# Kernel optimization log

Measured on AMD Instinct MI355X. Metric: run time of the kernel, lower is better.

The kernel has to match this reference:

```python
import jax, jax.numpy as jnp
import numpy as np

N_NODES = 20000
N_EDGES = 100000
NODE_IN = 16
EDGE_IN = 10
LEAK = 0.1
EPS = 1e-5


def setup_inputs() -> dict:
    key = jax.random.key(0)
    ks = iter(jax.random.split(key, 40))

    def rn(shape, scale):
        return jax.random.normal(next(ks), shape, dtype=jnp.float32) * scale

    inp = {}
    inp["x"] = jax.random.normal(next(ks), (N_NODES, NODE_IN), dtype=jnp.float32)
    inp["e"] = jax.random.normal(next(ks), (N_EDGES, EDGE_IN), dtype=jnp.float32)
    inp["edge_index"] = jax.random.randint(next(ks), (2, N_EDGES), 0, N_NODES, dtype=jnp.int64)
    inp["xbatch"] = jnp.zeros((N_NODES,), dtype=jnp.int64)

    # BatchNorm affine params
    inp["bn_node_g"] = jnp.ones((NODE_IN,), jnp.float32)
    inp["bn_node_b"] = jnp.zeros((NODE_IN,), jnp.float32)
    inp["bn_edge_g"] = jnp.ones((EDGE_IN,), jnp.float32)
    inp["bn_edge_b"] = jnp.zeros((EDGE_IN,), jnp.float32)

    # nn1: Lin(10,16) -> LeakyReLU -> Lin(16, 16*32) -> LeakyReLU
    inp["nn1_w1"] = rn((EDGE_IN, 16), 0.3); inp["nn1_b1"] = jnp.zeros((16,), jnp.float32)
    inp["nn1_w2"] = rn((16, 16 * 32), 0.25); inp["nn1_b2"] = jnp.zeros((16 * 32,), jnp.float32)
    # nn2: Lin(10,32) -> LeakyReLU -> Lin(32, 32*64) -> LeakyReLU
    inp["nn2_w1"] = rn((EDGE_IN, 32), 0.3); inp["nn2_b1"] = jnp.zeros((32,), jnp.float32)
    inp["nn2_w2"] = rn((32, 32 * 64), 0.18); inp["nn2_b2"] = jnp.zeros((32 * 64,), jnp.float32)

    # NNConv root weights + biases
    inp["l1_root"] = rn((16, 32), 0.25); inp["l1_bias"] = jnp.zeros((32,), jnp.float32)
    inp["l2_root"] = rn((32, 64), 0.18); inp["l2_bias"] = jnp.zeros((64,), jnp.float32)

    # edge_pred_mlp: 138 -> 64 -> 32 -> 16 -> 8 -> 2
    dims = [2 * 64 + EDGE_IN, 64, 32, 16, 8, 2]
    for i in range(5):
        inp[f"mlp_w{i+1}"] = rn((dims[i], dims[i + 1]), 1.0 / np.sqrt(dims[i]))
        inp[f"mlp_b{i+1}"] = jnp.zeros((dims[i + 1],), jnp.float32)
    return inp


def _bn(v, g, b):
    # BatchNorm1d, training-mode batch statistics (biased variance), eps=1e-5
    m = v.mean(axis=0)
    var = v.var(axis=0)
    return (v - m) * jax.lax.rsqrt(var + EPS) * g + b


def _lrelu(v):
    return jax.nn.leaky_relu(v, LEAK)


def _nnconv(x, src, dst, e, w1, b1, w2, b2, root, bias, c_in, c_out):
    # edge MLP -> per-edge weight matrix [E, c_in, c_out]
    h = _lrelu(e @ w1 + b1)
    W = _lrelu(h @ w2 + b2).reshape(-1, c_in, c_out)
    # gather source features, per-edge matmul, scatter-add to targets
    msg = jnp.einsum("ei,eio->eo", x[src], W)
    agg = jax.ops.segment_sum(msg, dst, num_segments=x.shape[0])
    return agg + x @ root + bias


def reference(x, e, edge_index, xbatch,
              bn_node_g, bn_node_b, bn_edge_g, bn_edge_b,
              nn1_w1, nn1_b1, nn1_w2, nn1_b2,
              nn2_w1, nn2_b1, nn2_w2, nn2_b2,
              l1_root, l1_bias, l2_root, l2_bias,
              mlp_w1, mlp_b1, mlp_w2, mlp_b2, mlp_w3, mlp_b3,
              mlp_w4, mlp_b4, mlp_w5, mlp_b5):
    src, dst = edge_index[0], edge_index[1]
    e = _bn(e, bn_edge_g, bn_edge_b)
    x = _bn(x, bn_node_g, bn_node_b)
    x = _nnconv(x, src, dst, e, nn1_w1, nn1_b1, nn1_w2, nn1_b2, l1_root, l1_bias, 16, 32)
    x = _nnconv(x, src, dst, e, nn2_w1, nn2_b1, nn2_w2, nn2_b2, l2_root, l2_bias, 32, 64)
    # MetaLayer edge model: cat(source, target, edge_attr) -> MLP -> [E, 2]
    h = jnp.concatenate([x[src], x[dst], e], axis=1)
    h = _lrelu(h @ mlp_w1 + mlp_b1)
    h = _lrelu(h @ mlp_w2 + mlp_b2)
    h = _lrelu(h @ mlp_w3 + mlp_b3)
    h = _lrelu(h @ mlp_w4 + mlp_b4)
    edge_pred = h @ mlp_w5 + mlp_b5
    return edge_pred
```

## Files before the change

kernel.cpp:

```cpp
#include <hip/hip_runtime.h>
#include <cstdint>

#define N_NODES 20000
#define N_EDGES 100000
#define BN_EPS 1e-5f

typedef __attribute__((ext_vector_type(8))) short short8;
typedef __attribute__((ext_vector_type(4))) float floatx4;
typedef __attribute__((ext_vector_type(2))) float float2v;

__device__ __forceinline__ float lrelu(float v) { return fmaxf(v, 0.1f * v); }
__device__ __forceinline__ float4 ld4(const float* p) { return *reinterpret_cast<const float4*>(p); }
__device__ __forceinline__ float2 ld2(const float* p) { return *reinterpret_cast<const float2*>(p); }

__device__ __forceinline__ void atomAddF(float* p, float v) {
#if defined(__HIP_DEVICE_COMPILE__)
    unsafeAtomicAdd(p, v);
#else
    atomicAdd(p, v);
#endif
}

__device__ __forceinline__ unsigned short f2bf(float f) {
    union { float f; uint32_t u; } v; v.f = f;
    uint32_t r = v.u + 0x7fffu + ((v.u >> 16) & 1u);
    return (unsigned short)(r >> 16);
}
__device__ __forceinline__ uint32_t pack2(float a, float b) {
    return (uint32_t)f2bf(a) | ((uint32_t)f2bf(b) << 16);
}
__device__ __forceinline__ short8 pack8(float4 a, float4 b) {
    union { short8 s; uint32_t u[4]; } r;
    r.u[0] = pack2(a.x, a.y); r.u[1] = pack2(a.z, a.w);
    r.u[2] = pack2(b.x, b.y); r.u[3] = pack2(b.z, b.w);
    return r.s;
}

__device__ void stats10_dev(const float* __restrict__ v, int rows, float* __restrict__ out,
                            int blk, int nblk, float* sh) {
    if (threadIdx.x < 20) sh[threadIdx.x] = 0.f;
    __syncthreads();
    int nf2 = rows * 5;
    int stride = nblk * 256;
    int g = blk * 256 + threadIdx.x;
    int c2 = g % 5;
    float s0 = 0.f, s1 = 0.f, q0 = 0.f, q1 = 0.f;
    const float2* p = reinterpret_cast<const float2*>(v);
    for (int i = g; i < nf2; i += stride) {
        float2 t = p[i];
        s0 += t.x; s1 += t.y; q0 += t.x * t.x; q1 += t.y * t.y;
    }
    atomicAdd(&sh[2 * c2], s0);
    atomicAdd(&sh[2 * c2 + 1], s1);
    atomicAdd(&sh[10 + 2 * c2], q0);
    atomicAdd(&sh[10 + 2 * c2 + 1], q1);
    __syncthreads();
    if (threadIdx.x < 20) atomAddF(&out[threadIdx.x], sh[threadIdx.x]);
}

__device__ void stats16_dev(const float* __restrict__ v, int rows, float* __restrict__ out,
                            int blk, int nblk, float* sh) {
    if (threadIdx.x < 32) sh[threadIdx.x] = 0.f;
    __syncthreads();
    int nf4 = rows * 4;
    int stride = nblk * 256;
    int g = blk * 256 + threadIdx.x;
    int cg = (g & 3) * 4;
    float s[4] = {0.f, 0.f, 0.f, 0.f}, q[4] = {0.f, 0.f, 0.f, 0.f};
    const float4* p = reinterpret_cast<const float4*>(v);
    for (int i = g; i < nf4; i += stride) {
        float4 t = p[i];
        s[0] += t.x; s[1] += t.y; s[2] += t.z; s[3] += t.w;
        q[0] += t.x * t.x; q[1] += t.y * t.y; q[2] += t.z * t.z; q[3] += t.w * t.w;
    }
    #pragma unroll
    for (int off = 32; off >= 4; off >>= 1) {
        #pragma unroll
        for (int j = 0; j < 4; ++j) {
            s[j] += __shfl_down(s[j], off, 64);
            q[j] += __shfl_down(q[j], off, 64);
        }
    }
    if ((threadIdx.x & 63) < 4) {
        #pragma unroll
        for (int j = 0; j < 4; ++j) {
            atomicAdd(&sh[cg + j], s[j]);
            atomicAdd(&sh[16 + cg + j], q[j]);
        }
    }
    __syncthreads();
    if (threadIdx.x < 32) atomAddF(&out[threadIdx.x], sh[threadIdx.x]);
}

template<int CIN, int COUT, int H, int OCH>
__device__ void convpack_row(const float* __restrict__ w2, const float* __restrict__ b2,
                             char* __restrict__ pk, int r) {
    constexpr int NROW = CIN * OCH;
    constexpr int WB = NROW * 64;
    constexpr int PACKB = WB + NROW * 4;
    if (r >= CIN * COUT) return;
    int chunk = r / NROW;
    int rem = r % NROW;
    int i = rem / OCH, ol = rem % OCH;
    int n = i * COUT + chunk * OCH + ol;
    char* base = pk + (size_t)chunk * PACKB;
    uint32_t pkv[16];
    #pragma unroll
    for (int t = 0; t < 16; ++t) pkv[t] = 0;
    #pragma unroll
    for (int k = 0; k < H; k += 2)
        pkv[k >> 1] = pack2(w2[(size_t)k * (CIN * COUT) + n],
                            w2[(size_t)(k + 1) * (CIN * COUT) + n]);
    uint4* ob = reinterpret_cast<uint4*>(base);
    #pragma unroll
    for (int q = 0; q < 4; ++q)
        ob[(size_t)q * NROW + rem] = make_uint4(pkv[4 * q], pkv[4 * q + 1],
                                                pkv[4 * q + 2], pkv[4 * q + 3]);
    ((float*)(base + WB))[rem] = b2[n];
}

#define P1_S10 120
#define P1_S16 120
__global__ __launch_bounds__(256)
void prep1_kernel(const float* __restrict__ e, const float* __restrict__ x,
                  float* __restrict__ stats_e, float* __restrict__ stats_x,
                  const int* __restrict__ dst, int* __restrict__ counts,
                  const float* __restrict__ nn1_w2, const float* __restrict__ nn1_b2, char* __restrict__ cpack1,
                  const float* __restrict__ nn2_w2, const float* __restrict__ nn2_b2, char* __restrict__ cpack2,
                  const float* __restrict__ mw1, unsigned short* __restrict__ w1t,
                  const float* __restrict__ mw2, const float* __restrict__ mb2,
                  const float* __restrict__ mw3, const float* __restrict__ mb3,
                  const float* __restrict__ mw4, const float* __restrict__ mb4,
                  const float* __restrict__ mw5, const float* __restrict__ mb5,
                  float* __restrict__ mlpw)
{
    __shared__ float sh[32];
    int b = blockIdx.x;
    if (b < P1_S10) {
        stats10_dev(e, N_EDGES, stats_e, b, P1_S10, sh);
    } else if (b < P1_S10 + P1_S16) {
        stats16_dev(x, N_NODES, stats_x, b - P1_S10, P1_S16, sh);
    } else if (b < 631) {
        int i = (b - 240) * 256 + threadIdx.x;
        if (i < N_EDGES) atomicAdd(&counts[dst[i]], 1);
    } else if (b < 633) {
        convpack_row<16, 32, 16, 32>(nn1_w2, nn1_b2, cpack1, (b - 631) * 256 + threadIdx.x);
    } else if (b < 641) {
        convpack_row<32, 64, 32, 16>(nn2_w2, nn2_b2, cpack2, (b - 633) * 256 + threadIdx.x);
    } else {
        if (threadIdx.x < 64) {
            int o = threadIdx.x;
            for (int k = 0; k < 160; k += 2) {
                float a = (k < 138) ? mw1[(size_t)k * 64 + o] : 0.f;
                float c = (k + 1 < 138) ? mw1[(size_t)(k + 1) * 64 + o] : 0.f;
                *reinterpret_cast<uint32_t*>(w1t + (size_t)o * 160 + k) = pack2(a, c);
            }
        }
        for (int i = threadIdx.x; i < 2764; i += 256) {
            float v = 0.f;
            if (i < 2048) v = mw2[i];
            else if (i < 2560) v = mw3[i - 2048];
            else if (i < 2688) v = mw4[i - 2560];
            else if (i < 2704) v = mw5[i - 2688];
            else if (i < 2736) v = mb2[i - 2704];
            else if (i < 2752) v = mb3[i - 2736];
            else if (i < 2760) v = mb4[i - 2752];
            else if (i < 2762) v = mb5[i - 2760];
            mlpw[i] = v;
        }
    }
}

__global__ void scan_kernel(const int* __restrict__ counts, int* __restrict__ starts,
                            int* __restrict__ cursor, int n) {
    __shared__ int wsum[4];
    const int CH = (n + 255) / 256;
    int t = threadIdx.x;
    int lane = t & 63, wv = t >> 6;
    int lo = t * CH, hi = min(lo + CH, n);
    int s = 0;
    for (int i = lo; i < hi; ++i) s += counts[i];
    int v = s;
    #pragma unroll
    for (int off = 1; off < 64; off <<= 1) {
        int u = __shfl_up(v, off, 64);
        if (lane >= off) v += u;
    }
    if (lane == 63) wsum[wv] = v;
    __syncthreads();
    int woff = 0;
    for (int w = 0; w < wv; ++w) woff += wsum[w];
    int acc = woff + v - s;
    for (int i = lo; i < hi; ++i) {
        starts[i] = acc; cursor[i] = acc; acc += counts[i];
    }
}

#define P2_N16 1250
#define P2_SCAT 391
#define P2_HGEN 391
__global__ __launch_bounds__(256)
void prep2_kernel(const float* __restrict__ x, const float* __restrict__ stats_x,
                  const float* __restrict__ bn_node_g, const float* __restrict__ bn_node_b,
                  float* __restrict__ x_n,
                  const int* __restrict__ dst, int* __restrict__ cursor, int* __restrict__ epos,
                  const float* __restrict__ e, const float* __restrict__ stats_e,
                  const float* __restrict__ bn_edge_g, const float* __restrict__ bn_edge_b,
                  float* __restrict__ e_n,
                  const float* __restrict__ w1a, const float* __restrict__ b1a,
                  const float* __restrict__ w1b, const float* __restrict__ b1b,
                  unsigned short* __restrict__ h1, unsigned short* __restrict__ h2)
{
    int b = blockIdx.x;
    if (b < P2_N16) {
        int idx = b * 256 + threadIdx.x;
        if (idx >= N_NODES * 16) return;
        int c = idx & 15;
        float N = (float)N_NODES;
        float m = stats_x[c] / N;
        float var = stats_x[16 + c] / N - m * m;
        float sc = rsqrtf(var + BN_EPS) * bn_node_g[c];
        x_n[idx] = (x[idx] - m) * sc + bn_node_b[c];
    } else if (b < P2_N16 + P2_SCAT) {
        int i = (b - P2_N16) * 256 + threadIdx.x;
        if (i < N_EDGES) {
            int p = atomicAdd(&cursor[dst[i]], 1);
            epos[i] = p;
        }
    } else {
        int eg = (b - P2_N16 - P2_SCAT) * 256 + threadIdx.x;
        if (eg >= N_EDGES) return;
        float ev[10];
        float Ecnt = (float)N_EDGES;
        #pragma unroll
        for (int j = 0; j < 10; ++j) {
            float m = stats_e[j] / Ecnt;
            float var = stats_e[10 + j] / Ecnt - m * m;
            float sc = rsqrtf(var + BN_EPS) * bn_edge_g[j];
            ev[j] = (e[(size_t)eg * 10 + j] - m) * sc + bn_edge_b[j];
            e_n[(size_t)eg * 10 + j] = ev[j];
        }
        {
            uint32_t pk[16];
            #pragma unroll
            for (int t = 0; t < 16; ++t) pk[t] = 0;
            #pragma unroll
            for (int k = 0; k < 16; k += 2) {
                float a0 = b1a[k], a1 = b1a[k + 1];
                #pragma unroll
                for (int j = 0; j < 10; ++j) {
                    a0 += ev[j] * w1a[j * 16 + k];
                    a1 += ev[j] * w1a[j * 16 + k + 1];
                }
                pk[k >> 1] = pack2(lrelu(a0), lrelu(a1));
            }
            uint4* o = reinterpret_cast<uint4*>(h1 + (size_t)eg * 32);
            o[0] = make_uint4(pk[0], pk[1], pk[2], pk[3]);
            o[1] = make_uint4(pk[4], pk[5], pk[6], pk[7]);
            o[2] = make_uint4(pk[8], pk[9], pk[10], pk[11]);
            o[3] = make_uint4(pk[12], pk[13], pk[14], pk[15]);
        }
        {
            uint32_t pk[16];
            #pragma unroll
            for (int k = 0; k < 32; k += 2) {
                float a0 = b1b[k], a1 = b1b[k + 1];
                #pragma unroll
                for (int j = 0; j < 10; ++j) {
                    a0 += ev[j] * w1b[j * 32 + k];
                    a1 += ev[j] * w1b[j * 32 + k + 1];
                }
                pk[k >> 1] = pack2(lrelu(a0), lrelu(a1));
            }
            uint4* o = reinterpret_cast<uint4*>(h2 + (size_t)eg * 32);
            o[0] = make_uint4(pk[0], pk[1], pk[2], pk[3]);
            o[1] = make_uint4(pk[4], pk[5], pk[6], pk[7]);
            o[2] = make_uint4(pk[8], pk[9], pk[10], pk[11]);
            o[3] = make_uint4(pk[12], pk[13], pk[14], pk[15]);
        }
    }
}

template<int CIN, int COUT, int OCH, int NE, int IB>
__global__ __launch_bounds__(256, 4)
void conv_lds_kernel(const unsigned short* __restrict__ hbuf,
                     const char* __restrict__ pack,
                     const int* __restrict__ src,
                     const int* __restrict__ epos,
                     const float* __restrict__ xin,
                     float* __restrict__ msgbuf,
                     int n_edges)
{
    constexpr int NCH = COUT / OCH;
    constexpr int NROW = CIN * OCH;
    constexpr int WB = NROW * 64;
    constexpr int PACKB = WB + NROW * 4;
    constexpr int NOT = OCH / 16;
    __shared__ char smem[PACKB];

    int tid = threadIdx.x;
    int chunk = blockIdx.x % NCH;
    int eblk = blockIdx.x / NCH;

    {
        const uint4* g = reinterpret_cast<const uint4*>(pack + (size_t)chunk * PACKB);
        uint4* s = reinterpret_cast<uint4*>(smem);
        #pragma unroll 1
        for (int o = tid; o < PACKB / 16; o += 256) s[o] = g[o];
    }
    __syncthreads();

    int wv = tid >> 6, lane = tid & 63;
    int el = lane & 15, quad = lane >> 4;
    int g0 = (eblk * 4 + wv) * NE;
    if (g0 * 16 >= n_edges) return;

    const unsigned short* wlds = reinterpret_cast<const unsigned short*>(smem)
                                 + ((size_t)quad * NROW + el) * 8;
    const float* blds = reinterpret_cast<const float*>(smem + WB) + quad * 4;

    int sg[NE], slot[NE];
    short8 bfrag[NE];
    #pragma unroll
    for (int g = 0; g < NE; ++g) {
        int e0 = (g0 + g) * 16;
        int e = (e0 < n_edges) ? (e0 + el) : el;
        sg[g] = src[e];
        slot[g] = epos[e];
        bfrag[g] = *reinterpret_cast<const short8*>(hbuf + (size_t)e * 32 + quad * 8);
    }

    float2v msg0[NE][NOT], msg1[NE][NOT];
    #pragma unroll
    for (int g = 0; g < NE; ++g)
        #pragma unroll
        for (int t = 0; t < NOT; ++t) {
            msg0[g][t] = (float2v){0.f, 0.f};
            msg1[g][t] = (float2v){0.f, 0.f};
        }

    const float2v pt = {0.1f, 0.1f};

    #pragma unroll 1
    for (int ib = 0; ib < CIN / IB; ++ib) {
        float xs[NE][IB];
        #pragma unroll
        for (int g = 0; g < NE; ++g) {
            #pragma unroll
            for (int t = 0; t < IB; t += 4) {
                float4 v = ld4(xin + (size_t)sg[g] * CIN + ib * IB + t);
                xs[g][t] = v.x; xs[g][t + 1] = v.y; xs[g][t + 2] = v.z; xs[g][t + 3] = v.w;
            }
        }
        #pragma unroll
        for (int ii = 0; ii < IB; ++ii) {
            int i = ib * IB + ii;
            #pragma unroll
            for (int ot = 0; ot < NOT; ++ot) {
                short8 af = *reinterpret_cast<const short8*>(wlds + (i * OCH + ot * 16) * 8);
                float4 bb = *reinterpret_cast<const float4*>(blds + i * OCH + ot * 16);
                floatx4 cinit = {bb.x, bb.y, bb.z, bb.w};
                #pragma unroll
                for (int g = 0; g < NE; ++g) {
                    floatx4 c = __builtin_amdgcn_mfma_f32_16x16x32_bf16(af, bfrag[g], cinit, 0, 0, 0);
                    float2v c0 = {c[0], c[1]}, c1 = {c[2], c[3]};
                    float2v m0 = __builtin_elementwise_max(c0, c0 * pt);
                    float2v m1 = __builtin_elementwise_max(c1, c1 * pt);
                    float2v xi2 = {xs[g][ii], xs[g][ii]};
                    msg0[g][ot] += xi2 * m0;
                    msg1[g][ot] += xi2 * m1;
                }
            }
        }
    }

    #pragma unroll
    for (int g = 0; g < NE; ++g) {
        if ((g0 + g) * 16 >= n_edges) break;
        float* orow = msgbuf + (size_t)slot[g] * COUT + chunk * OCH;
        #pragma unroll
        for (int ot = 0; ot < NOT; ++ot)
            *reinterpret_cast<float4*>(orow + ot * 16 + quad * 4) =
                make_float4(msg0[g][ot][0], msg0[g][ot][1], msg1[g][ot][0], msg1[g][ot][1]);
    }
}

template<int CIN, int C>
__global__ __launch_bounds__(256)
void gather_root_kernel(const float* __restrict__ xin, const float* __restrict__ w,
                        const float* __restrict__ bias,
                        const float* __restrict__ msg,
                        const int* __restrict__ starts, const int* __restrict__ counts,
                        float* __restrict__ xout, int nodes)
{
    constexpr int NPW = 64 / C;
    int wv = blockIdx.x * 4 + (threadIdx.x >> 6);
    int lane = threadIdx.x & 63;
    int node = wv * NPW + lane / C;
    int ch = lane % C;
    if (node >= nodes) return;
    float acc = bias[ch];
    const float* xrow = xin + (size_t)node * CIN;
    #pragma unroll
    for (int i = 0; i < CIN; ++i) acc += xrow[i] * w[i * C + ch];
    int s0 = starts[node], cnt = counts[node];
    const float* mrow = msg + (size_t)s0 * C + ch;
    int i = 0;
    for (; i + 3 < cnt; i += 4) {
        float m0 = mrow[(size_t)(i)     * C];
        float m1 = mrow[(size_t)(i + 1) * C];
        float m2 = mrow[(size_t)(i + 2) * C];
        float m3 = mrow[(size_t)(i + 3) * C];
        acc += (m0 + m1) + (m2 + m3);
    }
    for (; i < cnt; ++i) acc += mrow[(size_t)i * C];
    xout[(size_t)node * C + ch] = acc;
}

__global__ __launch_bounds__(256)
void mlp2_kernel(const float* __restrict__ x2, const float* __restrict__ e_n,
                 const int* __restrict__ src, const int* __restrict__ dst,
                 const unsigned short* __restrict__ w1t, const float* __restrict__ b1,
                 const float* __restrict__ mlpw,
                 float* __restrict__ out, int n_edges)
{
    __shared__ float wl[2764];
    __shared__ float a1t[4 * 1092];
    __shared__ float a2scr[4 * 528];

    int tid = threadIdx.x;
    {
        const uint4* g = reinterpret_cast<const uint4*>(mlpw);
        uint4* s = reinterpret_cast<uint4*>(wl);
        #pragma unroll 1
        for (int i = tid; i < 691; i += 256) s[i] = g[i];
    }

    int wv = tid >> 6, lane = tid & 63;
    int el = lane & 15, quad = lane >> 4;
    int e = blockIdx.x * 64 + wv * 16 + el;
    int eS = (e < n_edges) ? e : (n_edges - 1);
    int sN = src[eS], dN = dst[eS];

    short8 bf[5];
    {
        const float* rs = x2 + (size_t)sN * 64 + quad * 8;
        const float* rd = x2 + (size_t)dN * 64 + quad * 8;
        bf[0] = pack8(ld4(rs), ld4(rs + 4));
        bf[1] = pack8(ld4(rs + 32), ld4(rs + 36));
        bf[2] = pack8(ld4(rd), ld4(rd + 4));
        bf[3] = pack8(ld4(rd + 32), ld4(rd + 36));
        union { short8 s; uint32_t u[4]; } t;
        t.u[0] = t.u[1] = t.u[2] = t.u[3] = 0;
        const float* ep = e_n + (size_t)eS * 10;
        if (quad == 0) {
            float2 p0 = ld2(ep), p1 = ld2(ep + 2), p2 = ld2(ep + 4), p3 = ld2(ep + 6);
            t.u[0] = pack2(p0.x, p0.y); t.u[1] = pack2(p1.x, p1.y);
            t.u[2] = pack2(p2.x, p2.y); t.u[3] = pack2(p3.x, p3.y);
        } else if (quad == 1) {
            float2 p4 = ld2(ep + 8);
            t.u[0] = pack2(p4.x, p4.y);
        }
        bf[4] = t.s;
    }

    float* slab = &a1t[wv * 1092];
    {
        floatx4 acc[4];
        #pragma unroll
        for (int ot = 0; ot < 4; ++ot) {
            float4 bb = ld4(b1 + ot * 16 + quad * 4);
            acc[ot] = (floatx4){bb.x, bb.y, bb.z, bb.w};
        }
        #pragma unroll
        for (int ks = 0; ks < 5; ++ks) {
            #pragma unroll
            for (int ot = 0; ot < 4; ++ot) {
                short8 af = *reinterpret_cast<const short8*>(
                    w1t + (size_t)(ot * 16 + el) * 160 + ks * 32 + quad * 8);
                acc[ot] = __builtin_amdgcn_mfma_f32_16x16x32_bf16(af, bf[ks], acc[ot], 0, 0, 0);
            }
        }
        #pragma unroll
        for (int ot = 0; ot < 4; ++ot) {
            #pragma unroll
            for (int r = 0; r < 4; ++r)
                slab[(ot * 16 + quad * 4 + r) * 17 + el] = lrelu(acc[ot][r]);
        }
    }
    __syncthreads();

    const float* w2l = wl;            const float* w3l = wl + 2048;
    const float* w4l = wl + 2560;     const float* w5l = wl + 2688;
    const float* b2l = wl + 2704;     const float* b3l = wl + 2736;
    const float* b4l = wl + 2752;     const float* b5l = wl + 2760;
    float* a2s = &a2scr[wv * 528];
    float* a3s = slab;
    float* a4s = slab + 512;
    int p = quad;

    {
        float a2[8];
        #pragma unroll
        for (int j = 0; j < 8; ++j) a2[j] = b2l[p * 8 + j];
        #pragma unroll 4
        for (int i = 0; i < 64; ++i) {
            float ai = slab[i * 17 + el];
            #pragma unroll
            for (int j = 0; j < 8; ++j) a2[j] += ai * w2l[i * 32 + p * 8 + j];
        }
        #pragma unroll
        for (int j = 0; j < 8; ++j) a2s[el * 33 + p * 8 + j] = lrelu(a2[j]);
    }
    {
        float a3[4];
        #pragma unroll
        for (int j = 0; j < 4; ++j) a3[j] = b3l[p * 4 + j];
        #pragma unroll 4
        for (int i = 0; i < 32; ++i) {
            float ai = a2s[el * 33 + i];
            #pragma unroll
            for (int j = 0; j < 4; ++j) a3[j] += ai * w3l[i * 16 + p * 4 + j];
        }
        #pragma unroll
        for (int j = 0; j < 4; ++j) a3s[el * 17 + p * 4 + j] = lrelu(a3[j]);
    }
    {
        float a4[2];
        a4[0] = b4l[p * 2]; a4[1] = b4l[p * 2 + 1];
        #pragma unroll
        for (int i = 0; i < 16; ++i) {
            float ai = a3s[el * 17 + i];
            a4[0] += ai * w4l[i * 8 + p * 2];
            a4[1] += ai * w4l[i * 8 + p * 2 + 1];
        }
        a4s[el * 9 + p * 2]     = lrelu(a4[0]);
        a4s[el * 9 + p * 2 + 1] = lrelu(a4[1]);
    }
    if (p < 2) {
        float o = b5l[p];
        #pragma unroll
        for (int i = 0; i < 8; ++i) o += a4s[el * 9 + i] * w5l[i * 2 + p];
        if (e < n_edges) out[(size_t)e * 2 + p] = o;
    }
}

extern "C" void kernel_launch(void* const* d_in, const int* in_sizes, int n_in,
                              void* d_out, int out_size, void* d_ws, size_t ws_size,
                              hipStream_t stream)
{
    const float* x  = (const float*)d_in[0];
    const float* e  = (const float*)d_in[1];
    const int*   ei = (const int*)d_in[2];
    const float* bn_node_g = (const float*)d_in[4];
    const float* bn_node_b = (const float*)d_in[5];
    const float* bn_edge_g = (const float*)d_in[6];
    const float* bn_edge_b = (const float*)d_in[7];
    const float* nn1_w1 = (const float*)d_in[8];
    const float* nn1_b1 = (const float*)d_in[9];
    const float* nn1_w2 = (const float*)d_in[10];
    const float* nn1_b2 = (const float*)d_in[11];
    const float* nn2_w1 = (const float*)d_in[12];
    const float* nn2_b1 = (const float*)d_in[13];
    const float* nn2_w2 = (const float*)d_in[14];
    const float* nn2_b2 = (const float*)d_in[15];
    const float* l1_root = (const float*)d_in[16];
    const float* l1_bias = (const float*)d_in[17];
    const float* l2_root = (const float*)d_in[18];
    const float* l2_bias = (const float*)d_in[19];
    const float* mw1 = (const float*)d_in[20]; const float* mb1 = (const float*)d_in[21];
    const float* mw2 = (const float*)d_in[22]; const float* mb2 = (const float*)d_in[23];
    const float* mw3 = (const float*)d_in[24]; const float* mb3 = (const float*)d_in[25];
    const float* mw4 = (const float*)d_in[26]; const float* mb4 = (const float*)d_in[27];
    const float* mw5 = (const float*)d_in[28]; const float* mb5 = (const float*)d_in[29];

    const int* src = ei;
    const int* dst = ei + N_EDGES;

    float* ws = (float*)d_ws;
    float* stats_e = ws;
    float* stats_x = ws + 32;
    int* counts = (int*)(ws + 64);
    int* starts = counts + 20000;
    int* cursor = starts + 20000;
    int* epos   = cursor + 20000;
    float* e_n = ws + 64 + 160000;
    float* x_n = e_n + 1000000;
    float* x1  = x_n + 320000;
    float* x2  = x1 + 640000;
    float* msg = x2 + 1280000;
    unsigned short* h1   = (unsigned short*)(msg + 6400000);
    unsigned short* h2   = h1 + 3200000;
    unsigned short* w1t  = h2 + 3200000;
    char* cpack1 = (char*)(w1t + 10240);
    char* cpack2 = cpack1 + 34816;
    float* mlpw = (float*)(cpack2 + 4 * 34816);
    float* out = (float*)d_out;

    (void)hipMemsetAsync(d_ws, 0, (64 + 20000) * 4, stream);

    prep1_kernel<<<642, 256, 0, stream>>>(
        e, x, stats_e, stats_x, dst, counts,
        nn1_w2, nn1_b2, cpack1, nn2_w2, nn2_b2, cpack2,
        mw1, w1t, mw2, mb2, mw3, mb3, mw4, mb4, mw5, mb5, mlpw);

    scan_kernel<<<1, 256, 0, stream>>>(counts, starts, cursor, N_NODES);

    prep2_kernel<<<P2_N16 + P2_SCAT + P2_HGEN, 256, 0, stream>>>(
        x, stats_x, bn_node_g, bn_node_b, x_n,
        dst, cursor, epos,
        e, stats_e, bn_edge_g, bn_edge_b, e_n,
        nn1_w1, nn1_b1, nn2_w1, nn2_b1, h1, h2);

    const int NGRP = (N_EDGES + 15) / 16;
    const int CB = (NGRP + 15) / 16;

    conv_lds_kernel<16, 32, 32, 4, 4><<<CB, 256, 0, stream>>>(h1, cpack1, src, epos, x_n, msg, N_EDGES);
    gather_root_kernel<16, 32><<<(N_NODES / 2 + 3) / 4, 256, 0, stream>>>(
        x_n, l1_root, l1_bias, msg, starts, counts, x1, N_NODES);

    conv_lds_kernel<32, 64, 16, 4, 8><<<CB * 4, 256, 0, stream>>>(h2, cpack2, src, epos, x1, msg, N_EDGES);
    gather_root_kernel<32, 64><<<(N_NODES + 3) / 4, 256, 0, stream>>>(
        x1, l2_root, l2_bias, msg, starts, counts, x2, N_NODES);

    mlp2_kernel<<<(N_EDGES + 63) / 64, 256, 0, stream>>>(
        x2, e_n, src, dst, w1t, mb1, mlpw, out, N_EDGES);
}
```

Before: 331.3 us.

## Parallelize prefix scan across blocks and split edge-MLP hidden generation per thread

Replaces the single-block serial-chunk scan over node counts with a two-kernel multi-block scan (block sums, then per-block exclusive scan with a prefix over block sums), so the scan is spread across many CUs instead of one. It also doubles the h-generation threads in prep2 so each edge is handled by two threads, each computing half of the first-layer hidden units, which cuts per-thread serial work and register pressure. The trade-off is an extra kernel launch, redundant BN normalization per thread pair, and a new workspace offset for the block sums.

```diff
diff --git a/kernel.cpp b/kernel.cpp
--- a/kernel.cpp
+++ b/kernel.cpp
@@ -4,6 +4,7 @@
 #define N_NODES 20000
 #define N_EDGES 100000
 #define BN_EPS 1e-5f
+#define SCAN_BLKS 79
 
 typedef __attribute__((ext_vector_type(8))) short short8;
 typedef __attribute__((ext_vector_type(4))) float floatx4;
@@ -171,34 +172,48 @@
     }
 }
 
-__global__ void scan_kernel(const int* __restrict__ counts, int* __restrict__ starts,
-                            int* __restrict__ cursor, int n) {
-    __shared__ int wsum[4];
-    const int CH = (n + 255) / 256;
-    int t = threadIdx.x;
+__global__ __launch_bounds__(256)
+void scanA_kernel(const int* __restrict__ counts, int* __restrict__ bsum, int n) {
+    __shared__ int sh[4];
+    int b = blockIdx.x, t = threadIdx.x;
+    int i = b * 256 + t;
+    int v = (i < n) ? counts[i] : 0;
+    #pragma unroll
+    for (int off = 32; off > 0; off >>= 1) v += __shfl_down(v, off, 64);
+    if ((t & 63) == 0) sh[t >> 6] = v;
+    __syncthreads();
+    if (t == 0) bsum[b] = sh[0] + sh[1] + sh[2] + sh[3];
+}
+
+__global__ __launch_bounds__(256)
+void scanC_kernel(const int* __restrict__ counts, const int* __restrict__ bsum,
+                  int* __restrict__ starts, int* __restrict__ cursor, int n) {
+    __shared__ int ws[4];
+    __shared__ int bs[SCAN_BLKS];
+    int b = blockIdx.x, t = threadIdx.x;
+    if (t < SCAN_BLKS) bs[t] = bsum[t];
+    int i = b * 256 + t;
+    int val = (i < n) ? counts[i] : 0;
     int lane = t & 63, wv = t >> 6;
-    int lo = t * CH, hi = min(lo + CH, n);
-    int s = 0;
-    for (int i = lo; i < hi; ++i) s += counts[i];
-    int v = s;
+    int v = val;
     #pragma unroll
     for (int off = 1; off < 64; off <<= 1) {
         int u = __shfl_up(v, off, 64);
         if (lane >= off) v += u;
     }
-    if (lane == 63) wsum[wv] = v;
+    if (lane == 63) ws[wv] = v;
     __syncthreads();
     int woff = 0;
-    for (int w = 0; w < wv; ++w) woff += wsum[w];
-    int acc = woff + v - s;
-    for (int i = lo; i < hi; ++i) {
-        starts[i] = acc; cursor[i] = acc; acc += counts[i];
-    }
+    for (int w = 0; w < wv; ++w) woff += ws[w];
+    int boff = 0;
+    for (int w = 0; w < b; ++w) boff += bs[w];
+    int ex = boff + woff + v - val;
+    if (i < n) { starts[i] = ex; cursor[i] = ex; }
 }
 
 #define P2_N16 1250
 #define P2_SCAT 391
-#define P2_HGEN 391
+#define P2_HGEN 782
 __global__ __launch_bounds__(256)
 void prep2_kernel(const float* __restrict__ x, const float* __restrict__ stats_x,
                   const float* __restrict__ bn_node_g, const float* __restrict__ bn_node_b,
@@ -228,8 +243,9 @@
             epos[i] = p;
         }
     } else {
-        int eg = (b - P2_N16 - P2_SCAT) * 256 + threadIdx.x;
-        if (eg >= N_EDGES) return;
+        int g = (b - P2_N16 - P2_SCAT) * 256 + threadIdx.x;
+        if (g >= 2 * N_EDGES) return;
+        int eg = g >> 1, hh = g & 1;
         float ev[10];
         float Ecnt = (float)N_EDGES;
         #pragma unroll
@@ -238,45 +254,44 @@
             float var = stats_e[10 + j] / Ecnt - m * m;
             float sc = rsqrtf(var + BN_EPS) * bn_edge_g[j];
             ev[j] = (e[(size_t)eg * 10 + j] - m) * sc + bn_edge_b[j];
-            e_n[(size_t)eg * 10 + j] = ev[j];
+        }
+        if (hh == 0) {
+            #pragma unroll
+            for (int j = 0; j < 10; ++j) e_n[(size_t)eg * 10 + j] = ev[j];
         }
         {
-            uint32_t pk[16];
-            #pragma unroll
-            for (int t = 0; t < 16; ++t) pk[t] = 0;
-            #pragma unroll
-            for (int k = 0; k < 16; k += 2) {
+            uint32_t pk[4];
+            #pragma unroll
+            for (int pp = 0; pp < 4; ++pp) {
+                int k = (hh * 4 + pp) * 2;
                 float a0 = b1a[k], a1 = b1a[k + 1];
                 #pragma unroll
                 for (int j = 0; j < 10; ++j) {
                     a0 += ev[j] * w1a[j * 16 + k];
                     a1 += ev[j] * w1a[j * 16 + k + 1];
                 }
-                pk[k >> 1] = pack2(lrelu(a0), lrelu(a1));
+                pk[pp] = pack2(lrelu(a0), lrelu(a1));
             }
             uint4* o = reinterpret_cast<uint4*>(h1 + (size_t)eg * 32);
-            o[0] = make_uint4(pk[0], pk[1], pk[2], pk[3]);
-            o[1] = make_uint4(pk[4], pk[5], pk[6], pk[7]);
-            o[2] = make_uint4(pk[8], pk[9], pk[10], pk[11]);
-            o[3] = make_uint4(pk[12], pk[13], pk[14], pk[15]);
+            o[hh] = make_uint4(pk[0], pk[1], pk[2], pk[3]);
+            o[2 + hh] = make_uint4(0, 0, 0, 0);
         }
         {
-            uint32_t pk[16];
-            #pragma unroll
-            for (int k = 0; k < 32; k += 2) {
+            uint32_t pk[8];
+            #pragma unroll
+            for (int pp = 0; pp < 8; ++pp) {
+                int k = (hh * 8 + pp) * 2;
                 float a0 = b1b[k], a1 = b1b[k + 1];
                 #pragma unroll
                 for (int j = 0; j < 10; ++j) {
                     a0 += ev[j] * w1b[j * 32 + k];
                     a1 += ev[j] * w1b[j * 32 + k + 1];
                 }
-                pk[k >> 1] = pack2(lrelu(a0), lrelu(a1));
+                pk[pp] = pack2(lrelu(a0), lrelu(a1));
             }
             uint4* o = reinterpret_cast<uint4*>(h2 + (size_t)eg * 32);
-            o[0] = make_uint4(pk[0], pk[1], pk[2], pk[3]);
-            o[1] = make_uint4(pk[4], pk[5], pk[6], pk[7]);
-            o[2] = make_uint4(pk[8], pk[9], pk[10], pk[11]);
-            o[3] = make_uint4(pk[12], pk[13], pk[14], pk[15]);
+            o[hh * 2]     = make_uint4(pk[0], pk[1], pk[2], pk[3]);
+            o[hh * 2 + 1] = make_uint4(pk[4], pk[5], pk[6], pk[7]);
         }
     }
 }
@@ -584,7 +599,8 @@
     int* starts = counts + 20000;
     int* cursor = starts + 20000;
     int* epos   = cursor + 20000;
-    float* e_n = ws + 64 + 160000;
+    int* bsum   = epos + 100000;
+    float* e_n = ws + 64 + 160128;
     float* x_n = e_n + 1000000;
     float* x1  = x_n + 320000;
     float* x2  = x1 + 640000;
@@ -604,7 +620,8 @@
         nn1_w2, nn1_b2, cpack1, nn2_w2, nn2_b2, cpack2,
         mw1, w1t, mw2, mb2, mw3, mb3, mw4, mb4, mw5, mb5, mlpw);
 
-    scan_kernel<<<1, 256, 0, stream>>>(counts, starts, cursor, N_NODES);
+    scanA_kernel<<<SCAN_BLKS, 256, 0, stream>>>(counts, bsum, N_NODES);
+    scanC_kernel<<<SCAN_BLKS, 256, 0, stream>>>(counts, bsum, starts, cursor, N_NODES);
 
     prep2_kernel<<<P2_N16 + P2_SCAT + P2_HGEN, 256, 0, stream>>>(
         x, stats_x, bn_node_g, bn_node_b, x_n,
```

After: 272.0 us, median of 2. 1.22x faster.
